# Performance work log

Hardware: AMD Instinct MI355X
Metric: run time of the kernel (lower is better)

## Reference

```python
import jax, jax.numpy as jnp
import numpy as np

ELT_BATCH = 64            # number of candidate elements (rows)
OBS_PER_ELT = 100_000     # observations per element (uniform row_lengths)
DATA_SIZE = ELT_BATCH * OBS_PER_ELT
THRESH_DEG = 2.0
THRESH_HIT_PROB_POST = 0.95


def _deg2dist(deg):
    # chord length on unit sphere subtended by angle `deg`
    return 2.0 * np.sin(np.radians(deg) / 2.0)


def setup_inputs() -> dict:
    key = jax.random.key(0)
    k1, k2, k3, k4 = jax.random.split(key, 4)
    # observed unit directions
    u_obs = jax.random.normal(k1, (DATA_SIZE, 3), dtype=jnp.float32)
    u_obs = u_obs / jnp.linalg.norm(u_obs, axis=-1, keepdims=True)
    # predicted directions = observed + small perturbation so a realistic
    # fraction of observations fall inside the 2-degree threshold
    noise = 0.01 * jax.random.normal(k2, (DATA_SIZE, 3), dtype=jnp.float32)
    u_pred = u_obs + noise
    u_pred = u_pred / jnp.linalg.norm(u_pred, axis=-1, keepdims=True)
    # mixture-model params per element: hit fraction h in (0.1, 0.9), decay lam in (1, 10)
    h = 0.1 + 0.8 * jax.random.uniform(k3, (ELT_BATCH,), dtype=jnp.float32)
    lam = 1.0 + 9.0 * jax.random.uniform(k4, (ELT_BATCH,), dtype=jnp.float32)
    # squared chord-distance threshold per element (constant buffer in the layer)
    thresh_s2 = jnp.full((ELT_BATCH,), np.float32(_deg2dist(THRESH_DEG) ** 2), dtype=jnp.float32)
    return {"u_pred": u_pred, "u_obs": u_obs, "h": h, "lam": lam, "thresh_s2": thresh_s2}


def reference(u_pred, u_obs, h, lam, thresh_s2):
    B = thresh_s2.shape[0]
    n_per = u_pred.shape[0] // B  # uniform row_lengths
    seg_ids = jnp.repeat(jnp.arange(B, dtype=jnp.int32), n_per)  # [data_size]

    # squared chord distance per observation
    du = u_pred - u_obs                                # [N, 3]
    s2 = jnp.sum(jnp.square(du), axis=-1)              # [N]

    thresh_rep = jnp.repeat(thresh_s2, n_per)          # [N]
    h_rep = jnp.repeat(h, n_per)                       # [N]
    lam_rep = jnp.repeat(lam, n_per)                   # [N]

    is_close = s2 < thresh_rep                         # [N] bool
    v = s2 / thresh_rep                                # normalized squared distance in [0,1) where close

    # truncated-exponential mixture model
    emlx = jnp.exp(-lam_rep * v)
    p_hit_cond = emlx * lam_rep / (1.0 - jnp.exp(-lam_rep))
    p_hit = h_rep * p_hit_cond
    p = p_hit + (1.0 - h_rep)

    # mask instead of boolean_mask: excluded entries contribute 0 to segment sums
    log_p = jnp.where(is_close, jnp.log(p), 0.0)
    p_hit_post = p_hit / p
    is_real_hit = p_hit_post > THRESH_HIT_PROB_POST
    p_hit_filtered = jnp.where(is_close & is_real_hit, p_hit_post, 0.0)

    log_like = jax.ops.segment_sum(log_p, seg_ids, num_segments=B)        # [B]
    hits = jax.ops.segment_sum(p_hit_filtered, seg_ids, num_segments=B)   # [B]
    hits_raw = hits  # original code sums p_hit_filtered for both outputs
    return (log_like, hits, hits_raw)
```

## Files before the change

### kernel.cpp

```cpp
#include <hip/hip_runtime.h>


constexpr int ELT_BATCH     = 64;
constexpr int OBS_PER_ELT   = 100000;
constexpr int GROUPS_PER_SEG = OBS_PER_ELT / 4;
constexpr int F4_PER_SEG     = OBS_PER_ELT * 3 / 4;
constexpr int BLOCKS_PER_SEG = 32;
constexpr int BLOCK          = 256;

__device__ __forceinline__ float wave_reduce_sum(float v) {
    #pragma unroll
    for (int off = 32; off > 0; off >>= 1)
        v += __shfl_down(v, off, 64);
    return v;
}

__global__ __launch_bounds__(BLOCK) void TrajectoryScore_58145267253396_kernel(
    const float4* __restrict__ pred4,
    const float4* __restrict__ obs4,
    const float*  __restrict__ h_arr,
    const float*  __restrict__ lam_arr,
    const float*  __restrict__ th_arr,
    float*        __restrict__ out)
{
    const int seg        = blockIdx.x / BLOCKS_PER_SEG;
    const int blk_in_seg = blockIdx.x % BLOCKS_PER_SEG;
    const int tid        = threadIdx.x;

    const float h      = h_arr[seg];
    const float lam    = lam_arr[seg];
    const float th     = th_arr[seg];
    const float inv_th = 1.0f / th;
    const float coef   = h * lam / (1.0f - __expf(-lam));
    const float omh    = 1.0f - h;
    const float nli    = -lam * inv_th;

    float ll = 0.0f;
    float hs = 0.0f;

    const int seg_base = seg * F4_PER_SEG;

    for (int g = blk_in_seg * BLOCK + tid; g < GROUPS_PER_SEG; g += BLOCKS_PER_SEG * BLOCK) {
        const int base = seg_base + g * 3;
        const float4 a0 = pred4[base], a1 = pred4[base + 1], a2 = pred4[base + 2];
        const float4 b0 = obs4[base],  b1 = obs4[base + 1],  b2 = obs4[base + 2];

        float dx, dy, dz, s2[4];
        dx = a0.x - b0.x; dy = a0.y - b0.y; dz = a0.z - b0.z;
        s2[0] = dx * dx + dy * dy + dz * dz;
        dx = a0.w - b0.w; dy = a1.x - b1.x; dz = a1.y - b1.y;
        s2[1] = dx * dx + dy * dy + dz * dz;
        dx = a1.z - b1.z; dy = a1.w - b1.w; dz = a2.x - b2.x;
        s2[2] = dx * dx + dy * dy + dz * dz;
        dx = a2.y - b2.y; dy = a2.z - b2.z; dz = a2.w - b2.w;
        s2[3] = dx * dx + dy * dy + dz * dz;

        #pragma unroll
        for (int k = 0; k < 4; ++k) {
            const float s     = s2[k];
            const float e     = __expf(nli * s);
            const float p_hit = coef * e;
            const float p     = p_hit + omh;
            const bool  close = s < th;
            const float lp    = __logf(p);
            ll += close ? lp : 0.0f;
            const float post  = p_hit / p;
            hs += (close && post > 0.95f) ? post : 0.0f;
        }
    }

    ll = wave_reduce_sum(ll);
    hs = wave_reduce_sum(hs);

    __shared__ float sll[BLOCK / 64];
    __shared__ float shs[BLOCK / 64];
    const int wave = tid >> 6;
    const int lane = tid & 63;
    if (lane == 0) { sll[wave] = ll; shs[wave] = hs; }
    __syncthreads();
    if (tid == 0) {
        float L = 0.0f, H = 0.0f;
        #pragma unroll
        for (int w = 0; w < BLOCK / 64; ++w) { L += sll[w]; H += shs[w]; }
        atomicAdd(&out[seg], L);
        atomicAdd(&out[ELT_BATCH + seg], H);
        atomicAdd(&out[2 * ELT_BATCH + seg], H);
    }
}

extern "C" void kernel_launch(void* const* d_in, const int* in_sizes, int n_in,
                              void* d_out, int out_size, void* d_ws, size_t ws_size,
                              hipStream_t stream) {
    const float4* pred4  = (const float4*)d_in[0];
    const float4* obs4   = (const float4*)d_in[1];
    const float*  h_arr  = (const float*)d_in[2];
    const float*  lam_arr = (const float*)d_in[3];
    const float*  th_arr = (const float*)d_in[4];
    float* out = (float*)d_out;

    hipMemsetAsync(out, 0, out_size * sizeof(float), stream);

    dim3 grid(ELT_BATCH * BLOCKS_PER_SEG);
    dim3 block(BLOCK);
    TrajectoryScore_58145267253396_kernel<<<grid, block, 0, stream>>>(
        pred4, obs4, h_arr, lam_arr, th_arr, out);
}
```

Before: 178.9 us.

## Use coalesced per-lane float4 loads with shuffle-based observation reassembly

Each lane previously loaded three consecutive float4s, so neighbouring lanes read strided addresses. Now each wave takes a contiguous chunk of 63 float4s (84 observations), one float4 per lane, which gives fully coalesced loads. Each observation's squared distance is rebuilt from lane-residue patterns with a single shuffle, and the loop is unrolled four times to keep more loads in flight. The cost is extra shuffle and select work, one idle lane per chunk, and a tighter launch bound that limits registers per thread.

```diff
diff --git a/kernel.cpp b/kernel.cpp
--- a/kernel.cpp
+++ b/kernel.cpp
@@ -1,12 +1,16 @@
 #include <hip/hip_runtime.h>
 
 
-constexpr int ELT_BATCH     = 64;
-constexpr int OBS_PER_ELT   = 100000;
-constexpr int GROUPS_PER_SEG = OBS_PER_ELT / 4;
-constexpr int F4_PER_SEG     = OBS_PER_ELT * 3 / 4;
-constexpr int BLOCKS_PER_SEG = 32;
-constexpr int BLOCK          = 256;
+constexpr int ELT_BATCH       = 64;
+constexpr int OBS_PER_ELT     = 100000;
+constexpr int F4_PER_SEG      = OBS_PER_ELT * 3 / 4;
+constexpr int CHUNK_F4        = 63;
+constexpr int CHUNKS_PER_SEG  = (F4_PER_SEG + CHUNK_F4 - 1) / CHUNK_F4;
+constexpr int BLOCKS_PER_SEG  = 32;
+constexpr int BLOCK           = 256;
+constexpr int WAVES_PER_BLOCK = BLOCK / 64;
+constexpr int WAVES_PER_SEG   = BLOCKS_PER_SEG * WAVES_PER_BLOCK;
+constexpr int UNROLL          = 4;
 
 __device__ __forceinline__ float wave_reduce_sum(float v) {
     #pragma unroll
@@ -15,7 +19,7 @@
     return v;
 }
 
-__global__ __launch_bounds__(BLOCK) void TrajectoryScore_58145267253396_kernel(
+__global__ __launch_bounds__(BLOCK, 8) void TrajectoryScore_58145267253396_kernel(
     const float4* __restrict__ pred4,
     const float4* __restrict__ obs4,
     const float*  __restrict__ h_arr,
@@ -25,7 +29,10 @@
 {
     const int seg        = blockIdx.x / BLOCKS_PER_SEG;
     const int blk_in_seg = blockIdx.x % BLOCKS_PER_SEG;
-    const int tid        = threadIdx.x;
+    const int tid  = threadIdx.x;
+    const int lane = tid & 63;
+    const int wave = tid >> 6;
+    const int wseg = blk_in_seg * WAVES_PER_BLOCK + wave;
 
     const float h      = h_arr[seg];
     const float lam    = lam_arr[seg];
@@ -35,53 +42,83 @@
     const float omh    = 1.0f - h;
     const float nli    = -lam * inv_th;
 
+    const int  m  = lane % 3;
+    const bool m0 = (m == 0);
+    const bool m1 = (m == 1);
+
+    const int seg_f4 = seg * F4_PER_SEG;
+
     float ll = 0.0f;
     float hs = 0.0f;
 
-    const int seg_base = seg * F4_PER_SEG;
-
-    for (int g = blk_in_seg * BLOCK + tid; g < GROUPS_PER_SEG; g += BLOCKS_PER_SEG * BLOCK) {
-        const int base = seg_base + g * 3;
-        const float4 a0 = pred4[base], a1 = pred4[base + 1], a2 = pred4[base + 2];
-        const float4 b0 = obs4[base],  b1 = obs4[base + 1],  b2 = obs4[base + 2];
-
-        float dx, dy, dz, s2[4];
-        dx = a0.x - b0.x; dy = a0.y - b0.y; dz = a0.z - b0.z;
-        s2[0] = dx * dx + dy * dy + dz * dz;
-        dx = a0.w - b0.w; dy = a1.x - b1.x; dz = a1.y - b1.y;
-        s2[1] = dx * dx + dy * dy + dz * dz;
-        dx = a1.z - b1.z; dy = a1.w - b1.w; dz = a2.x - b2.x;
-        s2[2] = dx * dx + dy * dy + dz * dz;
-        dx = a2.y - b2.y; dy = a2.z - b2.z; dz = a2.w - b2.w;
-        s2[3] = dx * dx + dy * dy + dz * dz;
+    for (int c0 = wseg; c0 < CHUNKS_PER_SEG; c0 += UNROLL * WAVES_PER_SEG) {
+        float4 A[UNROLL], B[UNROLL];
+        int    act[UNROLL];
 
         #pragma unroll
-        for (int k = 0; k < 4; ++k) {
-            const float s     = s2[k];
-            const float e     = __expf(nli * s);
-            const float p_hit = coef * e;
-            const float p     = p_hit + omh;
-            const bool  close = s < th;
-            const float lp    = __logf(p);
-            ll += close ? lp : 0.0f;
-            const float post  = p_hit / p;
-            hs += (close && post > 0.95f) ? post : 0.0f;
+        for (int u = 0; u < UNROLL; ++u) {
+            const int c = c0 + u * WAVES_PER_SEG;
+            if (c < CHUNKS_PER_SEG) {
+                const int base = c * CHUNK_F4;
+                const int idx  = seg_f4 + min(base + lane, F4_PER_SEG - 1);
+                A[u]   = pred4[idx];
+                B[u]   = obs4[idx];
+                act[u] = min(CHUNK_F4, F4_PER_SEG - base);
+            } else {
+                act[u] = 0;
+            }
+        }
+
+        #pragma unroll
+        for (int u = 0; u < UNROLL; ++u) {
+            if (act[u] != 0) {
+                const float4 a = A[u], b = B[u];
+                const float d0 = a.x - b.x, d1 = a.y - b.y, d2 = a.z - b.z, d3 = a.w - b.w;
+                const float q0 = d0 * d0, q1 = d1 * d1, q2 = d2 * d2, q3 = d3 * d3;
+
+                const float head = m1 ? (q0 + q1) : q0;
+                const float hn   = __shfl_down(head, 1, 64);
+
+                const float t12 = q1 + q2;
+                const float s2A = m0 ? (q0 + t12) : (m1 ? (q2 + q3 + hn) : (t12 + q3));
+                const float s2B = q3 + hn;
+
+                const bool lv = lane < act[u];
+                {
+                    const float e  = __expf(nli * s2A);
+                    const float ph = coef * e;
+                    const float p  = ph + omh;
+                    const float lp = __logf(p);
+                    const float po = ph / p;
+                    const bool  cl = (s2A < th) && lv;
+                    ll += cl ? lp : 0.0f;
+                    hs += (cl && po > 0.95f) ? po : 0.0f;
+                }
+                {
+                    const float e  = __expf(nli * s2B);
+                    const float ph = coef * e;
+                    const float p  = ph + omh;
+                    const float lp = __logf(p);
+                    const float po = ph / p;
+                    const bool  cl = (s2B < th) && lv && m0;
+                    ll += cl ? lp : 0.0f;
+                    hs += (cl && po > 0.95f) ? po : 0.0f;
+                }
+            }
         }
     }
 
     ll = wave_reduce_sum(ll);
     hs = wave_reduce_sum(hs);
 
-    __shared__ float sll[BLOCK / 64];
-    __shared__ float shs[BLOCK / 64];
-    const int wave = tid >> 6;
-    const int lane = tid & 63;
+    __shared__ float sll[WAVES_PER_BLOCK];
+    __shared__ float shs[WAVES_PER_BLOCK];
     if (lane == 0) { sll[wave] = ll; shs[wave] = hs; }
     __syncthreads();
     if (tid == 0) {
         float L = 0.0f, H = 0.0f;
         #pragma unroll
-        for (int w = 0; w < BLOCK / 64; ++w) { L += sll[w]; H += shs[w]; }
+        for (int w = 0; w < WAVES_PER_BLOCK; ++w) { L += sll[w]; H += shs[w]; }
         atomicAdd(&out[seg], L);
         atomicAdd(&out[ELT_BATCH + seg], H);
         atomicAdd(&out[2 * ELT_BATCH + seg], H);
@@ -91,11 +128,11 @@
 extern "C" void kernel_launch(void* const* d_in, const int* in_sizes, int n_in,
                               void* d_out, int out_size, void* d_ws, size_t ws_size,
                               hipStream_t stream) {
-    const float4* pred4  = (const float4*)d_in[0];
-    const float4* obs4   = (const float4*)d_in[1];
-    const float*  h_arr  = (const float*)d_in[2];
+    const float4* pred4   = (const float4*)d_in[0];
+    const float4* obs4    = (const float4*)d_in[1];
+    const float*  h_arr   = (const float*)d_in[2];
     const float*  lam_arr = (const float*)d_in[3];
-    const float*  th_arr = (const float*)d_in[4];
+    const float*  th_arr  = (const float*)d_in[4];
     float* out = (float*)d_out;
 
     hipMemsetAsync(out, 0, out_size * sizeof(float), stream);
```

After: 179.4 us. Within noise of the previous version (+0.3%).
